# Kernel tuning notes

Hardware: AMD Instinct MI355X
Metric: run time of the kernel (lower is better)

Reference implementation:

```python
import jax, jax.numpy as jnp
import numpy as np

B, L, O, K, H = 8192, 128, 512, 8, 20  # batch, num_latent, num_obs, causes/node, hidden


def setup_inputs() -> dict:
    key = jax.random.key(0)
    ks = jax.random.split(key, 7)
    x = jax.random.normal(ks[0], (B, L), dtype=jnp.float32)
    # noise ~ Normal(0, 0.1), one scalar per (sample, observed node); noise_coeff = 1.0
    noise = 0.1 * jax.random.normal(ks[1], (B, O), dtype=jnp.float32)
    # latent-cause indices per observed node (fixed in-degree K)
    cause_idx = jax.random.randint(ks[2], (O, K), 0, L, dtype=jnp.int32)
    # per-node MLP weights: Linear(K+1,H) -> tanh -> Linear(H,H) -> tanh -> Linear(H,1)
    W1 = jax.random.normal(ks[3], (O, K + 1, H), dtype=jnp.float32) / np.sqrt(K + 1).astype(np.float32)
    b1 = jnp.zeros((O, H), dtype=jnp.float32)
    W2 = jax.random.normal(ks[4], (O, H, H), dtype=jnp.float32) / np.sqrt(H).astype(np.float32)
    b2 = jnp.zeros((O, H), dtype=jnp.float32)
    W3 = jax.random.normal(ks[5], (O, H), dtype=jnp.float32) / np.sqrt(H).astype(np.float32)
    b3 = jnp.zeros((O,), dtype=jnp.float32)
    return {"x": x, "noise": noise, "cause_idx": cause_idx,
            "W1": W1, "b1": b1, "W2": W2, "b2": b2, "W3": W3, "b3": b3}


def reference(x, noise, cause_idx, W1, b1, W2, b2, W3, b3):
    # Gather each observed node's latent causes: [B, O, K]
    gathered = x[:, cause_idx]
    # Prepend the noise column (torch.cat((noise, x_subset), axis=1)): [B, O, K+1]
    inp = jnp.concatenate([noise[..., None], gathered], axis=-1)
    # Per-node tiny MLP as grouped batched GEMMs
    h = jnp.tanh(jnp.einsum('boi,oih->boh', inp, W1) + b1)   # [B, O, H]
    h = jnp.tanh(jnp.einsum('boh,ohg->bog', h, W2) + b2)     # [B, O, H]
    out = jnp.einsum('boh,oh->bo', h, W3) + b3               # [B, O] (concat of per-node outputs)
    return out
```

## Files before the change

### kernel.cpp

```cpp
#include <hip/hip_runtime.h>
#include <hip/hip_bf16.h>

#define B_TOT 8192
#define O_DIM 512
#define L_DIM 128
#define K_DIM 8
#define H_DIM 20

#define TB 64
#define TO 8
#define NTH 256
#define XPITCH 66

typedef short bf16x8 __attribute__((ext_vector_type(8)));
typedef float f32x4  __attribute__((ext_vector_type(4)));

#define OFF_W2T 0
#define OFF_W1  20480
#define OFF_BB  29696
#define OFF_NS  32768
#define OFF_XT  35072
#define SMEM_BYTES 51968

__device__ __forceinline__ float fast_tanh(float x) {
    float e = __builtin_amdgcn_exp2f(x * 2.885390081777927f);
    float r = __builtin_amdgcn_rcpf(1.0f + e);
    return 1.0f - 2.0f * r;
}
__device__ __forceinline__ unsigned short f2bf(float f) {
    unsigned u = __float_as_uint(f);
    return (unsigned short)((u + 0x8000u) >> 16);
}

__global__ __launch_bounds__(NTH, 3) void medil_fused(
    const float* __restrict__ x, const float* __restrict__ noise,
    const int* __restrict__ cause_idx,
    const float* __restrict__ W1, const float* __restrict__ b1,
    const float* __restrict__ W2, const float* __restrict__ b2,
    const float* __restrict__ W3, const float* __restrict__ b3,
    float* __restrict__ out)
{
    __shared__ __align__(16) char smem[SMEM_BYTES];
    unsigned short* w2t = (unsigned short*)(smem + OFF_W2T);
    float*          w1s = (float*)(smem + OFF_W1);
    float*          bbs = (float*)(smem + OFF_BB);
    float*          nss = (float*)(smem + OFF_NS);
    unsigned short* xts = (unsigned short*)(smem + OFF_XT);

    const int tid = threadIdx.x;
    const int o0 = (blockIdx.x & 63) * TO;
    const int b0 = (blockIdx.x >> 6) * TB;

    {
        const int ol = tid >> 5, idx = tid & 31;
        unsigned int* w2z = (unsigned int*)(w2t + ol * 1280);
        #pragma unroll
        for (int z = 0; z < 20; ++z) w2z[idx + 32 * z] = 0u;
        float* w1o = w1s + ol * 288;
        #pragma unroll
        for (int z = 0; z < 9; ++z) w1o[idx + 32 * z] = 0.f;
        float* bbo = bbs + ol * 96;
        #pragma unroll
        for (int z = 0; z < 3; ++z) bbo[idx + 32 * z] = 0.f;
    }
    __syncthreads();
    {
        const int ol = tid >> 5, idx = tid & 31;
        const int o = o0 + ol;
        if (idx < 20) {
            unsigned short* w2o = w2t + ol * 1280;
            #pragma unroll
            for (int hi = 0; hi < 20; ++hi)
                w2o[idx * 40 + hi] = f2bf(W2[(size_t)o * 400 + hi * 20 + idx]);
            float* w1o = w1s + ol * 288;
            #pragma unroll
            for (int k = 0; k < 9; ++k)
                w1o[k * 32 + idx] = W1[(size_t)o * 180 + k * 20 + idx];
            float* bbo = bbs + ol * 96;
            bbo[idx]      = b1[o * H_DIM + idx];
            bbo[32 + idx] = b2[o * H_DIM + idx];
            bbo[64 + idx] = W3[o * H_DIM + idx];
        }
    }
    {
        const int r = tid >> 3, oln = tid & 7;
        nss[r * 9 + oln]        = noise[(size_t)(b0 + r) * O_DIM + o0 + oln];
        nss[(r + 32) * 9 + oln] = noise[(size_t)(b0 + r + 32) * O_DIM + o0 + oln];
    }
    {
        #pragma unroll
        for (int i = 0; i < 8; ++i) {
            int t = tid + NTH * i;
            int c4 = t & 31, r = t >> 5;
            float4 v = *(const float4*)(x + (size_t)(b0 + r) * L_DIM + 4 * c4);
            float vv[4] = {v.x, v.y, v.z, v.w};
            #pragma unroll
            for (int s = 0; s < 4; ++s) {
                int col = 4 * c4 + s;
                xts[col * XPITCH + (r ^ (col & 31))] = f2bf(vv[s]);
            }
        }
    }
    __syncthreads();

    const int lane = tid & 63;
    const int wv   = tid >> 6;
    const int l15  = lane & 15;
    const int q    = lane >> 4;

    #pragma unroll 1
    for (int oo = 0; oo < 2; ++oo) {
        const int ol = __builtin_amdgcn_readfirstlane(2 * wv + oo);
        const int o  = o0 + ol;

        float w1r[9][8];
        const float* w1o = w1s + ol * 288;
        #pragma unroll
        for (int k = 0; k < 9; ++k) {
            float4 lo = *(const float4*)(w1o + k * 32 + q * 8);
            float4 hi = *(const float4*)(w1o + k * 32 + q * 8 + 4);
            w1r[k][0] = lo.x; w1r[k][1] = lo.y; w1r[k][2] = lo.z; w1r[k][3] = lo.w;
            w1r[k][4] = hi.x; w1r[k][5] = hi.y; w1r[k][6] = hi.z; w1r[k][7] = hi.w;
        }
        const float* bbo = bbs + ol * 96;
        float b1r[8];
        {
            float4 lo = *(const float4*)(bbo + q * 8);
            float4 hi = *(const float4*)(bbo + q * 8 + 4);
            b1r[0] = lo.x; b1r[1] = lo.y; b1r[2] = lo.z; b1r[3] = lo.w;
            b1r[4] = hi.x; b1r[5] = hi.y; b1r[6] = hi.z; b1r[7] = hi.w;
        }
        float4 b2a = *(const float4*)(bbo + 32 + 4 * q);
        float4 b2b = *(const float4*)(bbo + 48 + 4 * q);
        float4 w3a = *(const float4*)(bbo + 64 + 4 * q);
        float4 w3b = *(const float4*)(bbo + 80 + 4 * q);
        bf16x8 a2a = *(const bf16x8*)(w2t + ol * 1280 + l15 * 40 + q * 8);
        bf16x8 a2b = *(const bf16x8*)(w2t + ol * 1280 + (16 + l15) * 40 + q * 8);
        int cols[8];
        {
            const int* cip = cause_idx + o * K_DIM;
            #pragma unroll
            for (int k = 0; k < 8; ++k) cols[k] = cip[k];
        }
        const float b3v = b3[o];

        #pragma unroll 1
        for (int bt = 0; bt < 4; ++bt) {
            const int row = bt * 16 + l15;
            float nz = nss[row * 9 + ol];
            float z[8];
            #pragma unroll
            for (int j = 0; j < 8; ++j) z[j] = fmaf(nz, w1r[0][j], b1r[j]);
            #pragma unroll
            for (int k = 0; k < 8; ++k) {
                int col = cols[k];
                unsigned short uh = xts[col * XPITCH + (row ^ (col & 31))];
                float xv = __uint_as_float(((unsigned)uh) << 16);
                #pragma unroll
                for (int j = 0; j < 8; ++j) z[j] = fmaf(xv, w1r[k + 1][j], z[j]);
            }
            union { bf16x8 v; unsigned int u[4]; } b2v;
            #pragma unroll
            for (int i = 0; i < 4; ++i) {
                float t0 = fast_tanh(z[2 * i]);
                float t1 = fast_tanh(z[2 * i + 1]);
                union { __hip_bfloat162 h; unsigned int u; } p;
                p.h = __float22bfloat162_rn(make_float2(t0, t1));
                b2v.u[i] = p.u;
            }
            f32x4 zero = {0.f, 0.f, 0.f, 0.f};
            f32x4 c2a = __builtin_amdgcn_mfma_f32_16x16x32_bf16(a2a, b2v.v, zero, 0, 0, 0);
            f32x4 c2b = __builtin_amdgcn_mfma_f32_16x16x32_bf16(a2b, b2v.v, zero, 0, 0, 0);
            float s = 0.f;
            s = fmaf(fast_tanh(c2a[0] + b2a.x), w3a.x, s);
            s = fmaf(fast_tanh(c2a[1] + b2a.y), w3a.y, s);
            s = fmaf(fast_tanh(c2a[2] + b2a.z), w3a.z, s);
            s = fmaf(fast_tanh(c2a[3] + b2a.w), w3a.w, s);
            s = fmaf(fast_tanh(c2b[0] + b2b.x), w3b.x, s);
            s = fmaf(fast_tanh(c2b[1] + b2b.y), w3b.y, s);
            s = fmaf(fast_tanh(c2b[2] + b2b.z), w3b.z, s);
            s = fmaf(fast_tanh(c2b[3] + b2b.w), w3b.w, s);
            s += __shfl_xor(s, 16);
            s += __shfl_xor(s, 32);
            s += b3v;
            if (lane < 16)
                out[(size_t)(b0 + row) * O_DIM + o] = s;
        }
    }
}

extern "C" void kernel_launch(void* const* d_in, const int* in_sizes, int n_in,
                              void* d_out, int out_size, void* d_ws, size_t ws_size,
                              hipStream_t stream) {
    const float* x         = (const float*)d_in[0];
    const float* noise     = (const float*)d_in[1];
    const int*   cause_idx = (const int*)d_in[2];
    const float* W1        = (const float*)d_in[3];
    const float* b1        = (const float*)d_in[4];
    const float* W2        = (const float*)d_in[5];
    const float* b2        = (const float*)d_in[6];
    const float* W3        = (const float*)d_in[7];
    const float* b3        = (const float*)d_in[8];
    float* out = (float*)d_out;

    dim3 grid((B_TOT / TB) * (O_DIM / TO));
    dim3 block(NTH);
    hipLaunchKernelGGL(medil_fused, grid, block, 0, stream,
                       x, noise, cause_idx, W1, b1, W2, b2, W3, b3, out);
}
```

Before: 201.2 us.

## Move layer-1 onto MFMA, repack smem layouts, stage outputs for coalesced stores

The first-layer 9x20 product moves from per-lane scalar FMAs onto bf16 MFMA instructions. The noise and gathered x values are packed into B fragments, and the layer-1 activations go through a per-wave LDS scratch buffer to become the layer-2 operand. The x tile is stored as packed bf16 pairs, W1 is pre-converted to bf16, and noise is stored as bf16. Outputs are staged in shared memory and written with coalesced float2 stores. This cuts VALU FMA work and register pressure, but adds LDS round trips and rounds W1 and noise to bf16, which lowers precision.

```diff
diff --git a/kernel.cpp b/kernel.cpp
--- a/kernel.cpp
+++ b/kernel.cpp
@@ -7,20 +7,24 @@
 #define K_DIM 8
 #define H_DIM 20
 
+#define TO 8
 #define TB 64
-#define TO 8
 #define NTH 256
-#define XPITCH 66
 
 typedef short bf16x8 __attribute__((ext_vector_type(8)));
 typedef float f32x4  __attribute__((ext_vector_type(4)));
 
-#define OFF_W2T 0
-#define OFF_W1  20480
-#define OFF_BB  29696
-#define OFF_NS  32768
-#define OFF_XT  35072
-#define SMEM_BYTES 51968
+#define OFF_XP  0
+#define OFF_W1T 16640
+#define OFF_W2T 24832
+#define OFF_BB  37120
+#define OFF_ZT  40192
+#define OFF_NS  45312
+#define OFF_OUT 46336
+#define SMEM_BYTES 48384
+
+#define ZERO_OFF OFF_W1T
+#define ZERO_DW  ((OFF_ZT + 5120 - OFF_W1T) / 4)
 
 __device__ __forceinline__ float fast_tanh(float x) {
     float e = __builtin_amdgcn_exp2f(x * 2.885390081777927f);
@@ -31,6 +35,12 @@
     unsigned u = __float_as_uint(f);
     return (unsigned short)((u + 0x8000u) >> 16);
 }
+__device__ __forceinline__ unsigned pkbf(float a, float b) {
+    union { __hip_bfloat162 h; unsigned u; } p;
+    p.h = __float22bfloat162_rn(make_float2(a, b));
+    return p.u;
+}
+union frag_u { uint4 u4; bf16x8 v; };
 
 __global__ __launch_bounds__(NTH, 3) void medil_fused(
     const float* __restrict__ x, const float* __restrict__ noise,
@@ -41,64 +51,49 @@
     float* __restrict__ out)
 {
     __shared__ __align__(16) char smem[SMEM_BYTES];
-    unsigned short* w2t = (unsigned short*)(smem + OFF_W2T);
-    float*          w1s = (float*)(smem + OFF_W1);
-    float*          bbs = (float*)(smem + OFF_BB);
-    float*          nss = (float*)(smem + OFF_NS);
-    unsigned short* xts = (unsigned short*)(smem + OFF_XT);
 
     const int tid = threadIdx.x;
     const int o0 = (blockIdx.x & 63) * TO;
     const int b0 = (blockIdx.x >> 6) * TB;
 
     {
-        const int ol = tid >> 5, idx = tid & 31;
-        unsigned int* w2z = (unsigned int*)(w2t + ol * 1280);
+        unsigned* z = (unsigned*)(smem + ZERO_OFF);
         #pragma unroll
-        for (int z = 0; z < 20; ++z) w2z[idx + 32 * z] = 0u;
-        float* w1o = w1s + ol * 288;
-        #pragma unroll
-        for (int z = 0; z < 9; ++z) w1o[idx + 32 * z] = 0.f;
-        float* bbo = bbs + ol * 96;
-        #pragma unroll
-        for (int z = 0; z < 3; ++z) bbo[idx + 32 * z] = 0.f;
+        for (int i = 0; i < ZERO_DW / NTH; ++i) z[tid + NTH * i] = 0u;
     }
     __syncthreads();
-    {
-        const int ol = tid >> 5, idx = tid & 31;
+
+    {
+        const int ol = tid >> 5, t32 = tid & 31;
         const int o = o0 + ol;
-        if (idx < 20) {
-            unsigned short* w2o = w2t + ol * 1280;
-            #pragma unroll
-            for (int hi = 0; hi < 20; ++hi)
-                w2o[idx * 40 + hi] = f2bf(W2[(size_t)o * 400 + hi * 20 + idx]);
-            float* w1o = w1s + ol * 288;
+        if (t32 < 20) {
+            unsigned short* w1t = (unsigned short*)(smem + OFF_W1T) + ol * 512;
             #pragma unroll
             for (int k = 0; k < 9; ++k)
-                w1o[k * 32 + idx] = W1[(size_t)o * 180 + k * 20 + idx];
-            float* bbo = bbs + ol * 96;
-            bbo[idx]      = b1[o * H_DIM + idx];
-            bbo[32 + idx] = b2[o * H_DIM + idx];
-            bbo[64 + idx] = W3[o * H_DIM + idx];
-        }
-    }
-    {
-        const int r = tid >> 3, oln = tid & 7;
-        nss[r * 9 + oln]        = noise[(size_t)(b0 + r) * O_DIM + o0 + oln];
-        nss[(r + 32) * 9 + oln] = noise[(size_t)(b0 + r + 32) * O_DIM + o0 + oln];
+                w1t[t32 * 16 + k] = f2bf(W1[(size_t)o * 180 + k * 20 + t32]);
+            unsigned short* w2t = (unsigned short*)(smem + OFF_W2T) + ol * 768;
+            #pragma unroll
+            for (int h = 0; h < 20; ++h)
+                w2t[t32 * 24 + h] = f2bf(W2[(size_t)o * 400 + h * 20 + t32]);
+            float* bb = (float*)(smem + OFF_BB) + ol * 96;
+            bb[t32]      = b1[o * H_DIM + t32];
+            bb[32 + t32] = b2[o * H_DIM + t32];
+            bb[64 + t32] = W3[o * H_DIM + t32];
+        }
+    }
+    {
+        const int b = tid >> 2, j = tid & 3;
+        float2 nv = *(const float2*)(noise + (size_t)(b0 + b) * O_DIM + o0 + 2 * j);
+        *(unsigned*)(smem + OFF_NS + b * 16 + j * 4) = pkbf(nv.x, nv.y);
     }
     {
         #pragma unroll
         for (int i = 0; i < 8; ++i) {
             int t = tid + NTH * i;
-            int c4 = t & 31, r = t >> 5;
+            int r = t >> 5, c4 = t & 31;
             float4 v = *(const float4*)(x + (size_t)(b0 + r) * L_DIM + 4 * c4);
-            float vv[4] = {v.x, v.y, v.z, v.w};
-            #pragma unroll
-            for (int s = 0; s < 4; ++s) {
-                int col = 4 * c4 + s;
-                xts[col * XPITCH + (r ^ (col & 31))] = f2bf(vv[s]);
-            }
+            *(unsigned*)(smem + OFF_XP + (2 * c4)     * 260 + r * 4) = pkbf(v.x, v.y);
+            *(unsigned*)(smem + OFF_XP + (2 * c4 + 1) * 260 + r * 4) = pkbf(v.z, v.w);
         }
     }
     __syncthreads();
@@ -107,85 +102,105 @@
     const int wv   = tid >> 6;
     const int l15  = lane & 15;
     const int q    = lane >> 4;
+    const bool q0 = (q == 0), q1 = (q == 1);
+    char* zt_w = smem + OFF_ZT + wv * 1280;
 
     #pragma unroll 1
     for (int oo = 0; oo < 2; ++oo) {
-        const int ol = __builtin_amdgcn_readfirstlane(2 * wv + oo);
+        const int ol = __builtin_amdgcn_readfirstlane(wv * 2 + oo);
         const int o  = o0 + ol;
 
-        float w1r[9][8];
-        const float* w1o = w1s + ol * 288;
-        #pragma unroll
-        for (int k = 0; k < 9; ++k) {
-            float4 lo = *(const float4*)(w1o + k * 32 + q * 8);
-            float4 hi = *(const float4*)(w1o + k * 32 + q * 8 + 4);
-            w1r[k][0] = lo.x; w1r[k][1] = lo.y; w1r[k][2] = lo.z; w1r[k][3] = lo.w;
-            w1r[k][4] = hi.x; w1r[k][5] = hi.y; w1r[k][6] = hi.z; w1r[k][7] = hi.w;
-        }
-        const float* bbo = bbs + ol * 96;
-        float b1r[8];
+        int c[8];
         {
-            float4 lo = *(const float4*)(bbo + q * 8);
-            float4 hi = *(const float4*)(bbo + q * 8 + 4);
-            b1r[0] = lo.x; b1r[1] = lo.y; b1r[2] = lo.z; b1r[3] = lo.w;
-            b1r[4] = hi.x; b1r[5] = hi.y; b1r[6] = hi.z; b1r[7] = hi.w;
-        }
-        float4 b2a = *(const float4*)(bbo + 32 + 4 * q);
-        float4 b2b = *(const float4*)(bbo + 48 + 4 * q);
-        float4 w3a = *(const float4*)(bbo + 64 + 4 * q);
-        float4 w3b = *(const float4*)(bbo + 80 + 4 * q);
-        bf16x8 a2a = *(const bf16x8*)(w2t + ol * 1280 + l15 * 40 + q * 8);
-        bf16x8 a2b = *(const bf16x8*)(w2t + ol * 1280 + (16 + l15) * 40 + q * 8);
-        int cols[8];
-        {
-            const int* cip = cause_idx + o * K_DIM;
-            #pragma unroll
-            for (int k = 0; k < 8; ++k) cols[k] = cip[k];
+            const int* cip = cause_idx + (size_t)o * K_DIM;
+            #pragma unroll
+            for (int k = 0; k < 8; ++k) c[k] = cip[k];
         }
         const float b3v = b3[o];
+
+        const int koff1 = (q & 1) * 16;
+        const int koff2 = (q < 2 ? q : 2) * 16;
+        frag_u a1a, a1b, a2a, a2b;
+        a1a.u4 = *(const uint4*)(smem + OFF_W1T + ol * 1024 + l15 * 32 + koff1);
+        a1b.u4 = *(const uint4*)(smem + OFF_W1T + ol * 1024 + (16 + l15) * 32 + koff1);
+        a2a.u4 = *(const uint4*)(smem + OFF_W2T + ol * 1536 + l15 * 48 + koff2);
+        a2b.u4 = *(const uint4*)(smem + OFF_W2T + ol * 1536 + (16 + l15) * 48 + koff2);
+
+        const float* bb = (const float*)(smem + OFF_BB) + ol * 96;
+        float4 b1q = *(const float4*)(bb + 4 * q);
+        float4 b1u = *(const float4*)(bb + 16);
+        float4 b2q = *(const float4*)(bb + 32 + 4 * q);
+        float4 b2u = *(const float4*)(bb + 48 + 4 * q);
+        float4 w3q = *(const float4*)(bb + 64 + 4 * q);
+        float4 w3u = *(const float4*)(bb + 80 + 4 * q);
 
         #pragma unroll 1
         for (int bt = 0; bt < 4; ++bt) {
-            const int row = bt * 16 + l15;
-            float nz = nss[row * 9 + ol];
-            float z[8];
-            #pragma unroll
-            for (int j = 0; j < 8; ++j) z[j] = fmaf(nz, w1r[0][j], b1r[j]);
+            const int brow = bt * 16 + l15;
+
+            unsigned xv[8];
             #pragma unroll
             for (int k = 0; k < 8; ++k) {
-                int col = cols[k];
-                unsigned short uh = xts[col * XPITCH + (row ^ (col & 31))];
-                float xv = __uint_as_float(((unsigned)uh) << 16);
-                #pragma unroll
-                for (int j = 0; j < 8; ++j) z[j] = fmaf(xv, w1r[k + 1][j], z[j]);
+                unsigned d = *(const unsigned*)(smem + OFF_XP + (c[k] >> 1) * 260 + brow * 4);
+                xv[k] = (d >> ((c[k] & 1) * 16)) & 0xFFFFu;
             }
-            union { bf16x8 v; unsigned int u[4]; } b2v;
-            #pragma unroll
-            for (int i = 0; i < 4; ++i) {
-                float t0 = fast_tanh(z[2 * i]);
-                float t1 = fast_tanh(z[2 * i + 1]);
-                union { __hip_bfloat162 h; unsigned int u; } p;
-                p.h = __float22bfloat162_rn(make_float2(t0, t1));
-                b2v.u[i] = p.u;
+            unsigned nz = *(const unsigned short*)(smem + OFF_NS + brow * 16 + ol * 2);
+            frag_u bf1;
+            bf1.u4.x = q0 ? (nz | (xv[0] << 16)) : (q1 ? xv[7] : 0u);
+            bf1.u4.y = q0 ? (xv[1] | (xv[2] << 16)) : 0u;
+            bf1.u4.z = q0 ? (xv[3] | (xv[4] << 16)) : 0u;
+            bf1.u4.w = q0 ? (xv[5] | (xv[6] << 16)) : 0u;
+
+            f32x4 zero = {0.f, 0.f, 0.f, 0.f};
+            f32x4 c1a = __builtin_amdgcn_mfma_f32_16x16x32_bf16(a1a.v, bf1.v, zero, 0, 0, 0);
+            f32x4 c1b = __builtin_amdgcn_mfma_f32_16x16x32_bf16(a1b.v, bf1.v, zero, 0, 0, 0);
+
+            __asm__ volatile("" ::: "memory");
+            {
+                float t0 = fast_tanh(c1a[0] + b1q.x);
+                float t1 = fast_tanh(c1a[1] + b1q.y);
+                float t2 = fast_tanh(c1a[2] + b1q.z);
+                float t3 = fast_tanh(c1a[3] + b1q.w);
+                uint2 pk = { pkbf(t0, t1), pkbf(t2, t3) };
+                *(uint2*)(zt_w + l15 * 80 + q * 8) = pk;
             }
-            f32x4 zero = {0.f, 0.f, 0.f, 0.f};
-            f32x4 c2a = __builtin_amdgcn_mfma_f32_16x16x32_bf16(a2a, b2v.v, zero, 0, 0, 0);
-            f32x4 c2b = __builtin_amdgcn_mfma_f32_16x16x32_bf16(a2b, b2v.v, zero, 0, 0, 0);
-            float s = 0.f;
-            s = fmaf(fast_tanh(c2a[0] + b2a.x), w3a.x, s);
-            s = fmaf(fast_tanh(c2a[1] + b2a.y), w3a.y, s);
-            s = fmaf(fast_tanh(c2a[2] + b2a.z), w3a.z, s);
-            s = fmaf(fast_tanh(c2a[3] + b2a.w), w3a.w, s);
-            s = fmaf(fast_tanh(c2b[0] + b2b.x), w3b.x, s);
-            s = fmaf(fast_tanh(c2b[1] + b2b.y), w3b.y, s);
-            s = fmaf(fast_tanh(c2b[2] + b2b.z), w3b.z, s);
-            s = fmaf(fast_tanh(c2b[3] + b2b.w), w3b.w, s);
+            if (q0) {
+                float t0 = fast_tanh(c1b[0] + b1u.x);
+                float t1 = fast_tanh(c1b[1] + b1u.y);
+                float t2 = fast_tanh(c1b[2] + b1u.z);
+                float t3 = fast_tanh(c1b[3] + b1u.w);
+                uint2 pk = { pkbf(t0, t1), pkbf(t2, t3) };
+                *(uint2*)(zt_w + l15 * 80 + 32) = pk;
+            }
+            __asm__ volatile("" ::: "memory");
+            frag_u bf2;
+            bf2.u4 = *(const uint4*)(zt_w + l15 * 80 + q * 16);
+
+            f32x4 c2a = __builtin_amdgcn_mfma_f32_16x16x32_bf16(a2a.v, bf2.v, zero, 0, 0, 0);
+            f32x4 c2b = __builtin_amdgcn_mfma_f32_16x16x32_bf16(a2b.v, bf2.v, zero, 0, 0, 0);
+
+            float s;
+            s = fast_tanh(c2a[0] + b2q.x) * w3q.x;
+            s = fmaf(fast_tanh(c2a[1] + b2q.y), w3q.y, s);
+            s = fmaf(fast_tanh(c2a[2] + b2q.z), w3q.z, s);
+            s = fmaf(fast_tanh(c2a[3] + b2q.w), w3q.w, s);
+            s = fmaf(fast_tanh(c2b[0] + b2u.x), w3u.x, s);
+            s = fmaf(fast_tanh(c2b[1] + b2u.y), w3u.y, s);
+            s = fmaf(fast_tanh(c2b[2] + b2u.z), w3u.z, s);
+            s = fmaf(fast_tanh(c2b[3] + b2u.w), w3u.w, s);
             s += __shfl_xor(s, 16);
             s += __shfl_xor(s, 32);
             s += b3v;
             if (lane < 16)
-                out[(size_t)(b0 + row) * O_DIM + o] = s;
-        }
+                *(float*)(smem + OFF_OUT + brow * 32 + ol * 4) = s;
+        }
+    }
+
+    __syncthreads();
+    {
+        const int b = tid >> 2, j = (tid & 3) * 2;
+        float2 v = *(const float2*)(smem + OFF_OUT + b * 32 + j * 4);
+        *(float2*)(out + (size_t)(b0 + b) * O_DIM + o0 + j) = v;
     }
 }
 
```

After: 194.9 us. 1.03x faster.
